# Kernel tuning notes

Hardware: AMD Instinct MI355X
Metric: run time of the kernel (lower is better)

Reference implementation:

```python
import jax, jax.numpy as jnp
import numpy as np

B = 256        # trees per batch
M = 1023       # nodes per tree (complete binary tree, depth 0..9)
N = B * M      # total flattened nodes
H = 128        # hidden dim
VOCAB = 100    # AST node-type vocab
NUM_CLASSES = 6
MAX_DEPTH = 10 # levels 0..9


def setup_inputs() -> dict:
    key = jax.random.key(0)
    k1, k2, k3, k4 = jax.random.split(key, 4)
    i = np.arange(M)
    parent_local = np.maximum((i - 1) // 2, 0)          # root points to itself
    depth_local = np.floor(np.log2(i + 1)).astype(np.int64)
    tree_off = np.arange(B, dtype=np.int64) * M
    parent_idx = (parent_local[None, :] + tree_off[:, None]).reshape(-1)
    depth = np.tile(depth_local, B)
    root_idx = tree_off
    return {
        "node_type": jax.random.randint(k1, (N,), 0, VOCAB, dtype=jnp.int64),
        "parent_idx": jnp.asarray(parent_idx),
        "depth": jnp.asarray(depth),
        "root_idx": jnp.asarray(root_idx),
        "E": jax.random.normal(k2, (VOCAB, H), dtype=jnp.float32) * 0.1,
        "Wh": jax.random.normal(k3, (H, H), dtype=jnp.float32) * (1.0 / np.sqrt(H)),
        "bh": jnp.zeros((H,), dtype=jnp.float32),
        "Wc": jax.random.normal(k4, (H, NUM_CLASSES), dtype=jnp.float32) * (1.0 / np.sqrt(H)),
        "bc": jnp.zeros((NUM_CLASSES,), dtype=jnp.float32),
    }


def reference(node_type, parent_idx, depth, root_idx, E, Wh, bh, Wc, bc):
    # Feature extraction: ast_class -> vector (Ast2VectorForPython analog)
    x = E[node_type]                         # [N, H]
    h = jnp.tanh(x)                          # leaves start from their own embedding
    # Leaf-to-root recursive propagation, one level at a time (children first).
    for d in range(MAX_DEPTH - 1, 0, -1):
        child_h = jnp.where((depth == d)[:, None], h, 0.0)
        agg = jax.ops.segment_sum(child_h, parent_idx, num_segments=N)  # [N, H]
        upd = jnp.tanh(x + agg @ Wh + bh)
        h = jnp.where((depth == d - 1)[:, None], upd, h)
    h_root = h[root_idx]                     # [B, H] == torch.stack(outputs, 0)
    logits = h_root @ Wc + bc                # nn.Linear(128, 6)
    return jax.nn.log_softmax(logits, axis=-1)
```

## Files before the change

### kernel.cpp

```cpp
#include <hip/hip_runtime.h>

#define TREES    256
#define MNODES   1023
#define HD       128
#define VOCAB_SZ 100
#define NCLS     6
#define NTHREADS 1024

typedef __attribute__((ext_vector_type(8))) short  short8;
typedef __attribute__((ext_vector_type(4))) unsigned short ushort4_t;
typedef __attribute__((ext_vector_type(8))) __bf16 bf16x8;
typedef __attribute__((ext_vector_type(4))) float  f32x4;

__device__ __forceinline__ unsigned short f2bf(float f) {
    unsigned int u = __float_as_uint(f);
    u += 0x7FFFu + ((u >> 16) & 1u);
    return (unsigned short)(u >> 16);
}
__device__ __forceinline__ float bf2f(unsigned short s) {
    return __uint_as_float(((unsigned int)s) << 16);
}
__device__ __forceinline__ float fast_tanh(float x) {
    float e = __expf(2.0f * x);
    return 1.0f - 2.0f / (e + 1.0f);
}

#define OFF_R1    0
#define OFF_WH    32768
#define OFF_GW    32768
#define OFF_BUFB  32768
#define OFF_ETBL  83968
#define OFF_NT    109568
#define OFF_BH    113664
#define OFF_HROOT 114176
#define LDS_BYTES 114688

__global__ __launch_bounds__(NTHREADS, 4)
void tree_rnn_kernel(const int* __restrict__ node_type,
                     const float* __restrict__ E,
                     const float* __restrict__ Wh,
                     const float* __restrict__ bh,
                     const float* __restrict__ Wc,
                     const float* __restrict__ bc,
                     float* __restrict__ out)
{
    __shared__ __align__(16) unsigned char lds[LDS_BYTES];
    int*   nt_lds = (int*)(lds + OFF_NT);
    float* bh_lds = (float*)(lds + OFF_BH);
    float* hroot  = (float*)(lds + OFF_HROOT);

    const int t    = blockIdx.x;
    const int tid  = threadIdx.x;
    const int lane = tid & 63;
    const int wv   = tid >> 6;
    const int l16  = lane & 15;
    const int lg   = lane >> 4;
    const int cw   = wv & 3;
    const int g    = wv >> 2;
    const int ncol0 = cw * 32 + l16;
    const int ncol1 = ncol0 + 16;

    if (tid < MNODES) nt_lds[tid] = node_type[t * MNODES + tid];
    if (tid < HD)     bh_lds[tid] = bh[tid];

    for (int i4 = tid; i4 < VOCAB_SZ * HD / 4; i4 += NTHREADS) {
        int row = i4 >> 5;
        int c4  = i4 & 31;
        float4 v = ((const float4*)E)[i4];
        ushort4_t e, te;
        e[0] = f2bf(v.x); e[1] = f2bf(v.y); e[2] = f2bf(v.z); e[3] = f2bf(v.w);
        te[0] = f2bf(fast_tanh(v.x)); te[1] = f2bf(fast_tanh(v.y));
        te[2] = f2bf(fast_tanh(v.z)); te[3] = f2bf(fast_tanh(v.w));
        int boff = row * 256 + ((c4 * 8) ^ ((row & 7) << 4));
        *(ushort4_t*)(lds + OFF_ETBL + boff) = e;
        *(ushort4_t*)(lds + OFF_R1   + boff) = te;
    }
    for (int i4 = tid; i4 < HD * HD / 4; i4 += NTHREADS) {
        int row = i4 >> 5;
        int c4  = i4 & 31;
        float4 v = ((const float4*)Wh)[i4];
        ushort4_t w;
        w[0] = f2bf(v.x); w[1] = f2bf(v.y); w[2] = f2bf(v.z); w[3] = f2bf(v.w);
        *(ushort4_t*)(lds + OFF_WH + row * 256 + ((c4 * 8) ^ ((row & 7) << 4))) = w;
    }
    __syncthreads();

    bf16x8 bfr[2][4];
    float  bhv[2];
    bhv[0] = bh_lds[ncol0];
    bhv[1] = bh_lds[ncol1];
    #pragma unroll
    for (int n = 0; n < 2; ++n) {
        int nc = (n == 0) ? ncol0 : ncol1;
        #pragma unroll
        for (int kt = 0; kt < 4; ++kt) {
            short8 s;
            #pragma unroll
            for (int i = 0; i < 8; ++i) {
                int krow = kt * 32 + lg * 8 + i;
                s[i] = *(const short*)(lds + OFF_WH + krow * 256 +
                                       ((nc * 2) ^ ((krow & 7) << 4)));
            }
            bfr[n][kt] = __builtin_bit_cast(bf16x8, s);
        }
    }
    __syncthreads();

    for (int mt = g; mt < 7; mt += 4) {
        int arow = mt * 16 + l16;
        bf16x8 a[4];
        #pragma unroll
        for (int kt = 0; kt < 4; ++kt) {
            short8 s = *(const short8*)(lds + OFF_R1 + arow * 256 +
                                        ((kt * 64 + lg * 16) ^ ((arow & 7) << 4)));
            a[kt] = __builtin_bit_cast(bf16x8, s);
        }
        f32x4 aA0 = {0,0,0,0}, aB0 = {0,0,0,0}, aA1 = {0,0,0,0}, aB1 = {0,0,0,0};
        aA0 = __builtin_amdgcn_mfma_f32_16x16x32_bf16(a[0], bfr[0][0], aA0, 0, 0, 0);
        aB0 = __builtin_amdgcn_mfma_f32_16x16x32_bf16(a[1], bfr[0][1], aB0, 0, 0, 0);
        aA1 = __builtin_amdgcn_mfma_f32_16x16x32_bf16(a[0], bfr[1][0], aA1, 0, 0, 0);
        aB1 = __builtin_amdgcn_mfma_f32_16x16x32_bf16(a[1], bfr[1][1], aB1, 0, 0, 0);
        aA0 = __builtin_amdgcn_mfma_f32_16x16x32_bf16(a[2], bfr[0][2], aA0, 0, 0, 0);
        aB0 = __builtin_amdgcn_mfma_f32_16x16x32_bf16(a[3], bfr[0][3], aB0, 0, 0, 0);
        aA1 = __builtin_amdgcn_mfma_f32_16x16x32_bf16(a[2], bfr[1][2], aA1, 0, 0, 0);
        aB1 = __builtin_amdgcn_mfma_f32_16x16x32_bf16(a[3], bfr[1][3], aB1, 0, 0, 0);
        f32x4 acc0 = aA0 + aB0;
        f32x4 acc1 = aA1 + aB1;
        #pragma unroll
        for (int r = 0; r < 4; ++r) {
            int prow = mt * 16 + lg * 4 + r;
            if (prow < VOCAB_SZ) {
                *(float*)(lds + OFF_GW + prow * 512 + ((ncol0 * 4) ^ ((prow & 7) << 4))) = acc0[r];
                *(float*)(lds + OFF_GW + prow * 512 + ((ncol1 * 4) ^ ((prow & 7) << 4))) = acc1[r];
            }
        }
    }
    __syncthreads();

    #pragma unroll
    for (int it = 0; it < 2; ++it) {
        int idx = it * NTHREADS + tid;
        int j   = idx >> 4;
        int c8  = idx & 15;
        int colb = c8 * 16;
        int tyP0 = nt_lds[255 + 2 * j], tyP1 = nt_lds[256 + 2 * j];
        int tyA0 = nt_lds[511 + 4 * j], tyA1 = nt_lds[512 + 4 * j];
        int tyB0 = nt_lds[513 + 4 * j], tyB1 = nt_lds[514 + 4 * j];
        short8 e0 = *(const short8*)(lds + OFF_ETBL + tyP0 * 256 + (colb ^ ((tyP0 & 7) << 4)));
        short8 e1 = *(const short8*)(lds + OFF_ETBL + tyP1 * 256 + (colb ^ ((tyP1 & 7) << 4)));
        float ga[8], gb[8];
        *(float4*)(ga)     = *(const float4*)(lds + OFF_GW + tyA0 * 512 + ((c8 * 32)      ^ ((tyA0 & 7) << 4)));
        *(float4*)(ga + 4) = *(const float4*)(lds + OFF_GW + tyA0 * 512 + ((c8 * 32 + 16) ^ ((tyA0 & 7) << 4)));
        float gt[8];
        *(float4*)(gt)     = *(const float4*)(lds + OFF_GW + tyA1 * 512 + ((c8 * 32)      ^ ((tyA1 & 7) << 4)));
        *(float4*)(gt + 4) = *(const float4*)(lds + OFF_GW + tyA1 * 512 + ((c8 * 32 + 16) ^ ((tyA1 & 7) << 4)));
        #pragma unroll
        for (int u = 0; u < 8; ++u) ga[u] += gt[u];
        *(float4*)(gb)     = *(const float4*)(lds + OFF_GW + tyB0 * 512 + ((c8 * 32)      ^ ((tyB0 & 7) << 4)));
        *(float4*)(gb + 4) = *(const float4*)(lds + OFF_GW + tyB0 * 512 + ((c8 * 32 + 16) ^ ((tyB0 & 7) << 4)));
        *(float4*)(gt)     = *(const float4*)(lds + OFF_GW + tyB1 * 512 + ((c8 * 32)      ^ ((tyB1 & 7) << 4)));
        *(float4*)(gt + 4) = *(const float4*)(lds + OFF_GW + tyB1 * 512 + ((c8 * 32 + 16) ^ ((tyB1 & 7) << 4)));
        #pragma unroll
        for (int u = 0; u < 8; ++u) gb[u] += gt[u];
        short8 o;
        #pragma unroll
        for (int u = 0; u < 8; ++u) {
            float b  = bh_lds[c8 * 8 + u];
            float h0 = fast_tanh(bf2f((unsigned short)e0[u]) + ga[u] + b);
            float h1 = fast_tanh(bf2f((unsigned short)e1[u]) + gb[u] + b);
            o[u] = (short)f2bf(h0 + h1);
        }
        *(short8*)(lds + OFF_R1 + j * 256 + (colb ^ ((j & 7) << 4))) = o;
    }
    __syncthreads();

    unsigned char* bin  = lds + OFF_R1;
    unsigned char* bout = lds + OFF_BUFB;
    for (int L = 7; L >= 0; --L) {
        const int P      = 1 << L;
        const int Loff   = P - 1;
        const int mtiles = (P + 15) >> 4;
        for (int mt = g; mt < mtiles; mt += 4) {
            int arow = mt * 16 + l16;
            bf16x8 a[4];
            #pragma unroll
            for (int kt = 0; kt < 4; ++kt) {
                short8 s = *(const short8*)(bin + arow * 256 +
                                            ((kt * 64 + lg * 16) ^ ((arow & 7) << 4)));
                a[kt] = __builtin_bit_cast(bf16x8, s);
            }
            f32x4 aA0 = {0,0,0,0}, aB0 = {0,0,0,0}, aA1 = {0,0,0,0}, aB1 = {0,0,0,0};
            aA0 = __builtin_amdgcn_mfma_f32_16x16x32_bf16(a[0], bfr[0][0], aA0, 0, 0, 0);
            aB0 = __builtin_amdgcn_mfma_f32_16x16x32_bf16(a[1], bfr[0][1], aB0, 0, 0, 0);
            aA1 = __builtin_amdgcn_mfma_f32_16x16x32_bf16(a[0], bfr[1][0], aA1, 0, 0, 0);
            aB1 = __builtin_amdgcn_mfma_f32_16x16x32_bf16(a[1], bfr[1][1], aB1, 0, 0, 0);
            aA0 = __builtin_amdgcn_mfma_f32_16x16x32_bf16(a[2], bfr[0][2], aA0, 0, 0, 0);
            aB0 = __builtin_amdgcn_mfma_f32_16x16x32_bf16(a[3], bfr[0][3], aB0, 0, 0, 0);
            aA1 = __builtin_amdgcn_mfma_f32_16x16x32_bf16(a[2], bfr[1][2], aA1, 0, 0, 0);
            aB1 = __builtin_amdgcn_mfma_f32_16x16x32_bf16(a[3], bfr[1][3], aB1, 0, 0, 0);
            f32x4 acc0 = aA0 + aB0;
            f32x4 acc1 = aA1 + aB1;
            float hp0 = 0.f, hp1 = 0.f;
            #pragma unroll
            for (int r = 0; r < 4; ++r) {
                int prow = mt * 16 + lg * 4 + r;
                if (prow < P) {
                    int ty   = nt_lds[Loff + prow];
                    float x0 = bf2f(*(const unsigned short*)
                                    (lds + OFF_ETBL + ty * 256 + ((ncol0 * 2) ^ ((ty & 7) << 4))));
                    float x1 = bf2f(*(const unsigned short*)
                                    (lds + OFF_ETBL + ty * 256 + ((ncol1 * 2) ^ ((ty & 7) << 4))));
                    float h0 = fast_tanh(x0 + acc0[r] + bhv[0]);
                    float h1 = fast_tanh(x1 + acc1[r] + bhv[1]);
                    if (L == 0) {
                        hroot[ncol0] = h0;
                        hroot[ncol1] = h1;
                    } else if (r & 1) {
                        int orow = prow >> 1;
                        *(short*)(bout + orow * 256 + ((ncol0 * 2) ^ ((orow & 7) << 4))) =
                            (short)f2bf(hp0 + h0);
                        *(short*)(bout + orow * 256 + ((ncol1 * 2) ^ ((orow & 7) << 4))) =
                            (short)f2bf(hp1 + h1);
                    } else {
                        hp0 = h0; hp1 = h1;
                    }
                }
            }
        }
        __syncthreads();
        unsigned char* tmp = bin; bin = bout; bout = tmp;
    }

    if (tid < 64) {
        float hA = hroot[tid];
        float hB = hroot[tid + 64];
        float lgt[NCLS];
        #pragma unroll
        for (int c = 0; c < NCLS; ++c) {
            float v = hA * Wc[tid * NCLS + c] + hB * Wc[(tid + 64) * NCLS + c];
            #pragma unroll
            for (int off = 32; off > 0; off >>= 1)
                v += __shfl_xor(v, off, 64);
            lgt[c] = v + bc[c];
        }
        if (tid == 0) {
            float mx = lgt[0];
            #pragma unroll
            for (int c = 1; c < NCLS; ++c) mx = fmaxf(mx, lgt[c]);
            float s = 0.f;
            #pragma unroll
            for (int c = 0; c < NCLS; ++c) s += __expf(lgt[c] - mx);
            float lse = mx + __logf(s);
            #pragma unroll
            for (int c = 0; c < NCLS; ++c) out[t * NCLS + c] = lgt[c] - lse;
        }
    }
}

extern "C" void kernel_launch(void* const* d_in, const int* in_sizes, int n_in,
                              void* d_out, int out_size, void* d_ws, size_t ws_size,
                              hipStream_t stream) {
    const int*   node_type = (const int*)d_in[0];
    const float* E  = (const float*)d_in[4];
    const float* Wh = (const float*)d_in[5];
    const float* bh = (const float*)d_in[6];
    const float* Wc = (const float*)d_in[7];
    const float* bc = (const float*)d_in[8];
    float* out = (float*)d_out;
    tree_rnn_kernel<<<dim3(TREES), dim3(NTHREADS), 0, stream>>>(node_type, E, Wh, bh, Wc, bc, out);
}
```

Measured before the change: 30.07 us.

## Split each tree into two half-subtree blocks plus a small root kernel

Each tree is now handled by two 512-thread blocks, one per root child subtree, instead of one 1024-thread block. Each block writes its subtree-root hidden state to workspace, and a second 64-thread kernel combines them, computes the root update, the classifier and the log-softmax. The change also stores the precomputed E@Wh table in bf16 to shrink LDS, and loads Wh fragments directly from global memory instead of staging them through LDS. The aim is more blocks, lower LDS per block and better occupancy. The cost is a second launch, a global round trip, a serial fp32 root matvec, and extra bf16 rounding of the table.

```diff
diff --git a/kernel.cpp b/kernel.cpp
--- a/kernel.cpp
+++ b/kernel.cpp
@@ -5,7 +5,7 @@
 #define HD       128
 #define VOCAB_SZ 100
 #define NCLS     6
-#define NTHREADS 1024
+#define K1_THREADS 512
 
 typedef __attribute__((ext_vector_type(8))) short  short8;
 typedef __attribute__((ext_vector_type(4))) unsigned short ushort4_t;
@@ -26,30 +26,26 @@
 }
 
 #define OFF_R1    0
-#define OFF_WH    32768
-#define OFF_GW    32768
-#define OFF_BUFB  32768
-#define OFF_ETBL  83968
-#define OFF_NT    109568
-#define OFF_BH    113664
-#define OFF_HROOT 114176
-#define LDS_BYTES 114688
-
-__global__ __launch_bounds__(NTHREADS, 4)
-void tree_rnn_kernel(const int* __restrict__ node_type,
-                     const float* __restrict__ E,
-                     const float* __restrict__ Wh,
-                     const float* __restrict__ bh,
-                     const float* __restrict__ Wc,
-                     const float* __restrict__ bc,
-                     float* __restrict__ out)
+#define OFF_GW    25600
+#define OFF_ETBL  51200
+#define OFF_NT    76800
+#define OFF_BH    80896
+#define LDS1      81408
+
+__global__ __launch_bounds__(K1_THREADS, 4)
+void k1_subtree(const int* __restrict__ node_type,
+                const float* __restrict__ E,
+                const float* __restrict__ Wh,
+                const float* __restrict__ bh,
+                float* __restrict__ ws)
 {
-    __shared__ __align__(16) unsigned char lds[LDS_BYTES];
+    __shared__ __align__(16) unsigned char lds[LDS1];
     int*   nt_lds = (int*)(lds + OFF_NT);
     float* bh_lds = (float*)(lds + OFF_BH);
-    float* hroot  = (float*)(lds + OFF_HROOT);
-
-    const int t    = blockIdx.x;
+
+    const int b    = blockIdx.x;
+    const int t    = b >> 1;
+    const int s    = b & 1;
     const int tid  = threadIdx.x;
     const int lane = tid & 63;
     const int wv   = tid >> 6;
@@ -60,10 +56,9 @@
     const int ncol0 = cw * 32 + l16;
     const int ncol1 = ncol0 + 16;
 
-    if (tid < MNODES) nt_lds[tid] = node_type[t * MNODES + tid];
-    if (tid < HD)     bh_lds[tid] = bh[tid];
-
-    for (int i4 = tid; i4 < VOCAB_SZ * HD / 4; i4 += NTHREADS) {
+    for (int i = tid; i < MNODES; i += K1_THREADS) nt_lds[i] = node_type[t * MNODES + i];
+    if (tid < HD) bh_lds[tid] = bh[tid];
+    for (int i4 = tid; i4 < VOCAB_SZ * HD / 4; i4 += K1_THREADS) {
         int row = i4 >> 5;
         int c4  = i4 & 31;
         float4 v = ((const float4*)E)[i4];
@@ -75,45 +70,34 @@
         *(ushort4_t*)(lds + OFF_ETBL + boff) = e;
         *(ushort4_t*)(lds + OFF_R1   + boff) = te;
     }
-    for (int i4 = tid; i4 < HD * HD / 4; i4 += NTHREADS) {
-        int row = i4 >> 5;
-        int c4  = i4 & 31;
-        float4 v = ((const float4*)Wh)[i4];
-        ushort4_t w;
-        w[0] = f2bf(v.x); w[1] = f2bf(v.y); w[2] = f2bf(v.z); w[3] = f2bf(v.w);
-        *(ushort4_t*)(lds + OFF_WH + row * 256 + ((c4 * 8) ^ ((row & 7) << 4))) = w;
-    }
-    __syncthreads();
 
     bf16x8 bfr[2][4];
-    float  bhv[2];
-    bhv[0] = bh_lds[ncol0];
-    bhv[1] = bh_lds[ncol1];
     #pragma unroll
     for (int n = 0; n < 2; ++n) {
         int nc = (n == 0) ? ncol0 : ncol1;
         #pragma unroll
         for (int kt = 0; kt < 4; ++kt) {
-            short8 s;
+            short8 sv;
             #pragma unroll
             for (int i = 0; i < 8; ++i) {
                 int krow = kt * 32 + lg * 8 + i;
-                s[i] = *(const short*)(lds + OFF_WH + krow * 256 +
-                                       ((nc * 2) ^ ((krow & 7) << 4)));
-            }
-            bfr[n][kt] = __builtin_bit_cast(bf16x8, s);
-        }
-    }
-    __syncthreads();
-
-    for (int mt = g; mt < 7; mt += 4) {
+                sv[i] = (short)f2bf(Wh[krow * HD + nc]);
+            }
+            bfr[n][kt] = __builtin_bit_cast(bf16x8, sv);
+        }
+    }
+    __syncthreads();
+    const float bhv0 = bh_lds[ncol0];
+    const float bhv1 = bh_lds[ncol1];
+
+    for (int mt = g; mt < 7; mt += 2) {
         int arow = mt * 16 + l16;
         bf16x8 a[4];
         #pragma unroll
         for (int kt = 0; kt < 4; ++kt) {
-            short8 s = *(const short8*)(lds + OFF_R1 + arow * 256 +
-                                        ((kt * 64 + lg * 16) ^ ((arow & 7) << 4)));
-            a[kt] = __builtin_bit_cast(bf16x8, s);
+            short8 sv = *(const short8*)(lds + OFF_R1 + arow * 256 +
+                                         ((kt * 64 + lg * 16) ^ ((arow & 7) << 4)));
+            a[kt] = __builtin_bit_cast(bf16x8, sv);
         }
         f32x4 aA0 = {0,0,0,0}, aB0 = {0,0,0,0}, aA1 = {0,0,0,0}, aB1 = {0,0,0,0};
         aA0 = __builtin_amdgcn_mfma_f32_16x16x32_bf16(a[0], bfr[0][0], aA0, 0, 0, 0);
@@ -130,64 +114,60 @@
         for (int r = 0; r < 4; ++r) {
             int prow = mt * 16 + lg * 4 + r;
             if (prow < VOCAB_SZ) {
-                *(float*)(lds + OFF_GW + prow * 512 + ((ncol0 * 4) ^ ((prow & 7) << 4))) = acc0[r];
-                *(float*)(lds + OFF_GW + prow * 512 + ((ncol1 * 4) ^ ((prow & 7) << 4))) = acc1[r];
-            }
-        }
-    }
-    __syncthreads();
-
+                *(short*)(lds + OFF_GW + prow * 256 + ((ncol0 * 2) ^ ((prow & 7) << 4))) =
+                    (short)f2bf(acc0[r]);
+                *(short*)(lds + OFF_GW + prow * 256 + ((ncol1 * 2) ^ ((prow & 7) << 4))) =
+                    (short)f2bf(acc1[r]);
+            }
+        }
+    }
+    __syncthreads();
+
+    const int G7 = 255 + s * 128;
+    const int G8 = 511 + s * 256;
     #pragma unroll
     for (int it = 0; it < 2; ++it) {
-        int idx = it * NTHREADS + tid;
-        int j   = idx >> 4;
+        int idx = it * K1_THREADS + tid;
+        int p   = idx >> 4;
         int c8  = idx & 15;
         int colb = c8 * 16;
-        int tyP0 = nt_lds[255 + 2 * j], tyP1 = nt_lds[256 + 2 * j];
-        int tyA0 = nt_lds[511 + 4 * j], tyA1 = nt_lds[512 + 4 * j];
-        int tyB0 = nt_lds[513 + 4 * j], tyB1 = nt_lds[514 + 4 * j];
-        short8 e0 = *(const short8*)(lds + OFF_ETBL + tyP0 * 256 + (colb ^ ((tyP0 & 7) << 4)));
-        short8 e1 = *(const short8*)(lds + OFF_ETBL + tyP1 * 256 + (colb ^ ((tyP1 & 7) << 4)));
-        float ga[8], gb[8];
-        *(float4*)(ga)     = *(const float4*)(lds + OFF_GW + tyA0 * 512 + ((c8 * 32)      ^ ((tyA0 & 7) << 4)));
-        *(float4*)(ga + 4) = *(const float4*)(lds + OFF_GW + tyA0 * 512 + ((c8 * 32 + 16) ^ ((tyA0 & 7) << 4)));
-        float gt[8];
-        *(float4*)(gt)     = *(const float4*)(lds + OFF_GW + tyA1 * 512 + ((c8 * 32)      ^ ((tyA1 & 7) << 4)));
-        *(float4*)(gt + 4) = *(const float4*)(lds + OFF_GW + tyA1 * 512 + ((c8 * 32 + 16) ^ ((tyA1 & 7) << 4)));
-        #pragma unroll
-        for (int u = 0; u < 8; ++u) ga[u] += gt[u];
-        *(float4*)(gb)     = *(const float4*)(lds + OFF_GW + tyB0 * 512 + ((c8 * 32)      ^ ((tyB0 & 7) << 4)));
-        *(float4*)(gb + 4) = *(const float4*)(lds + OFF_GW + tyB0 * 512 + ((c8 * 32 + 16) ^ ((tyB0 & 7) << 4)));
-        *(float4*)(gt)     = *(const float4*)(lds + OFF_GW + tyB1 * 512 + ((c8 * 32)      ^ ((tyB1 & 7) << 4)));
-        *(float4*)(gt + 4) = *(const float4*)(lds + OFF_GW + tyB1 * 512 + ((c8 * 32 + 16) ^ ((tyB1 & 7) << 4)));
-        #pragma unroll
-        for (int u = 0; u < 8; ++u) gb[u] += gt[u];
+        int tyP0 = nt_lds[G7 + 2 * p],     tyP1 = nt_lds[G7 + 2 * p + 1];
+        int tyA0 = nt_lds[G8 + 4 * p],     tyA1 = nt_lds[G8 + 4 * p + 1];
+        int tyB0 = nt_lds[G8 + 4 * p + 2], tyB1 = nt_lds[G8 + 4 * p + 3];
+        short8 e0  = *(const short8*)(lds + OFF_ETBL + tyP0 * 256 + (colb ^ ((tyP0 & 7) << 4)));
+        short8 e1  = *(const short8*)(lds + OFF_ETBL + tyP1 * 256 + (colb ^ ((tyP1 & 7) << 4)));
+        short8 g00 = *(const short8*)(lds + OFF_GW   + tyA0 * 256 + (colb ^ ((tyA0 & 7) << 4)));
+        short8 g01 = *(const short8*)(lds + OFF_GW   + tyA1 * 256 + (colb ^ ((tyA1 & 7) << 4)));
+        short8 g10 = *(const short8*)(lds + OFF_GW   + tyB0 * 256 + (colb ^ ((tyB0 & 7) << 4)));
+        short8 g11 = *(const short8*)(lds + OFF_GW   + tyB1 * 256 + (colb ^ ((tyB1 & 7) << 4)));
         short8 o;
         #pragma unroll
         for (int u = 0; u < 8; ++u) {
-            float b  = bh_lds[c8 * 8 + u];
-            float h0 = fast_tanh(bf2f((unsigned short)e0[u]) + ga[u] + b);
-            float h1 = fast_tanh(bf2f((unsigned short)e1[u]) + gb[u] + b);
+            float bb = bh_lds[c8 * 8 + u];
+            float h0 = fast_tanh(bf2f((unsigned short)e0[u]) + bf2f((unsigned short)g00[u]) +
+                                 bf2f((unsigned short)g01[u]) + bb);
+            float h1 = fast_tanh(bf2f((unsigned short)e1[u]) + bf2f((unsigned short)g10[u]) +
+                                 bf2f((unsigned short)g11[u]) + bb);
             o[u] = (short)f2bf(h0 + h1);
         }
-        *(short8*)(lds + OFF_R1 + j * 256 + (colb ^ ((j & 7) << 4))) = o;
+        *(short8*)(lds + OFF_R1 + p * 256 + (colb ^ ((p & 7) << 4))) = o;
     }
     __syncthreads();
 
     unsigned char* bin  = lds + OFF_R1;
-    unsigned char* bout = lds + OFF_BUFB;
-    for (int L = 7; L >= 0; --L) {
-        const int P      = 1 << L;
-        const int Loff   = P - 1;
+    unsigned char* bout = lds + OFF_GW;
+    for (int lam = 6; lam >= 0; --lam) {
+        const int P      = 1 << lam;
+        const int Gl     = 2 * P - 1 + s * P;
         const int mtiles = (P + 15) >> 4;
-        for (int mt = g; mt < mtiles; mt += 4) {
+        for (int mt = g; mt < mtiles; mt += 2) {
             int arow = mt * 16 + l16;
             bf16x8 a[4];
             #pragma unroll
             for (int kt = 0; kt < 4; ++kt) {
-                short8 s = *(const short8*)(bin + arow * 256 +
-                                            ((kt * 64 + lg * 16) ^ ((arow & 7) << 4)));
-                a[kt] = __builtin_bit_cast(bf16x8, s);
+                short8 sv = *(const short8*)(bin + arow * 256 +
+                                             ((kt * 64 + lg * 16) ^ ((arow & 7) << 4)));
+                a[kt] = __builtin_bit_cast(bf16x8, sv);
             }
             f32x4 aA0 = {0,0,0,0}, aB0 = {0,0,0,0}, aA1 = {0,0,0,0}, aB1 = {0,0,0,0};
             aA0 = __builtin_amdgcn_mfma_f32_16x16x32_bf16(a[0], bfr[0][0], aA0, 0, 0, 0);
@@ -205,16 +185,16 @@
             for (int r = 0; r < 4; ++r) {
                 int prow = mt * 16 + lg * 4 + r;
                 if (prow < P) {
-                    int ty   = nt_lds[Loff + prow];
+                    int ty   = nt_lds[Gl + prow];
                     float x0 = bf2f(*(const unsigned short*)
                                     (lds + OFF_ETBL + ty * 256 + ((ncol0 * 2) ^ ((ty & 7) << 4))));
                     float x1 = bf2f(*(const unsigned short*)
                                     (lds + OFF_ETBL + ty * 256 + ((ncol1 * 2) ^ ((ty & 7) << 4))));
-                    float h0 = fast_tanh(x0 + acc0[r] + bhv[0]);
-                    float h1 = fast_tanh(x1 + acc1[r] + bhv[1]);
-                    if (L == 0) {
-                        hroot[ncol0] = h0;
-                        hroot[ncol1] = h1;
+                    float h0 = fast_tanh(x0 + acc0[r] + bhv0);
+                    float h1 = fast_tanh(x1 + acc1[r] + bhv1);
+                    if (lam == 0) {
+                        ws[(t * 2 + s) * HD + ncol0] = h0;
+                        ws[(t * 2 + s) * HD + ncol1] = h1;
                     } else if (r & 1) {
                         int orow = prow >> 1;
                         *(short*)(bout + orow * 256 + ((ncol0 * 2) ^ ((orow & 7) << 4))) =
@@ -230,30 +210,57 @@
         __syncthreads();
         unsigned char* tmp = bin; bin = bout; bout = tmp;
     }
-
-    if (tid < 64) {
-        float hA = hroot[tid];
-        float hB = hroot[tid + 64];
-        float lgt[NCLS];
-        #pragma unroll
-        for (int c = 0; c < NCLS; ++c) {
-            float v = hA * Wc[tid * NCLS + c] + hB * Wc[(tid + 64) * NCLS + c];
-            #pragma unroll
-            for (int off = 32; off > 0; off >>= 1)
-                v += __shfl_xor(v, off, 64);
-            lgt[c] = v + bc[c];
-        }
-        if (tid == 0) {
-            float mx = lgt[0];
-            #pragma unroll
-            for (int c = 1; c < NCLS; ++c) mx = fmaxf(mx, lgt[c]);
-            float s = 0.f;
-            #pragma unroll
-            for (int c = 0; c < NCLS; ++c) s += __expf(lgt[c] - mx);
-            float lse = mx + __logf(s);
-            #pragma unroll
-            for (int c = 0; c < NCLS; ++c) out[t * NCLS + c] = lgt[c] - lse;
-        }
+}
+
+__global__ __launch_bounds__(64)
+void k2_root(const int* __restrict__ node_type,
+             const float* __restrict__ E,
+             const float* __restrict__ Wh,
+             const float* __restrict__ bh,
+             const float* __restrict__ Wc,
+             const float* __restrict__ bc,
+             const float* __restrict__ ws,
+             float* __restrict__ out)
+{
+    __shared__ float agg[HD];
+    const int t    = blockIdx.x;
+    const int lane = threadIdx.x;
+
+    const float* w0 = ws + t * 2 * HD;
+    agg[lane]      = w0[lane]      + w0[HD + lane];
+    agg[lane + 64] = w0[lane + 64] + w0[HD + lane + 64];
+    __syncthreads();
+
+    float x0 = 0.f, x1 = 0.f;
+    #pragma unroll 8
+    for (int k = 0; k < HD; ++k) {
+        float a = agg[k];
+        x0 += a * Wh[k * HD + lane];
+        x1 += a * Wh[k * HD + lane + 64];
+    }
+    int ty = node_type[t * MNODES];
+    float h0 = fast_tanh(E[ty * HD + lane]      + x0 + bh[lane]);
+    float h1 = fast_tanh(E[ty * HD + lane + 64] + x1 + bh[lane + 64]);
+
+    float lgt[NCLS];
+    #pragma unroll
+    for (int c = 0; c < NCLS; ++c) {
+        float v = h0 * Wc[lane * NCLS + c] + h1 * Wc[(lane + 64) * NCLS + c];
+        #pragma unroll
+        for (int off = 32; off > 0; off >>= 1)
+            v += __shfl_xor(v, off, 64);
+        lgt[c] = v + bc[c];
+    }
+    if (lane == 0) {
+        float mx = lgt[0];
+        #pragma unroll
+        for (int c = 1; c < NCLS; ++c) mx = fmaxf(mx, lgt[c]);
+        float sum = 0.f;
+        #pragma unroll
+        for (int c = 0; c < NCLS; ++c) sum += __expf(lgt[c] - mx);
+        float lse = mx + __logf(sum);
+        #pragma unroll
+        for (int c = 0; c < NCLS; ++c) out[t * NCLS + c] = lgt[c] - lse;
     }
 }
 
@@ -267,5 +274,8 @@
     const float* Wc = (const float*)d_in[7];
     const float* bc = (const float*)d_in[8];
     float* out = (float*)d_out;
-    tree_rnn_kernel<<<dim3(TREES), dim3(NTHREADS), 0, stream>>>(node_type, E, Wh, bh, Wc, bc, out);
-}
+    float* ws  = (float*)d_ws;
+
+    k1_subtree<<<dim3(TREES * 2), dim3(K1_THREADS), 0, stream>>>(node_type, E, Wh, bh, ws);
+    k2_root   <<<dim3(TREES),     dim3(64),         0, stream>>>(node_type, E, Wh, bh, Wc, bc, ws, out);
+}
```

Result: slower. 36.81 us (+22.4%).
